# Performance work log

Measured on AMD Instinct MI355X. Metric: run time of the kernel, lower is better.

Reference implementation:

```python
import jax, jax.numpy as jnp
import numpy as np

NUM_CLASSES = 80
NUM_ANCHORS = 3
CONF_TH = 0.5
IOU_TH = 0.4
INPUT_H = 416
INPUT_W = 416
# anchors[i] used for scale i (scale1=stride8, scale2=stride16, scale3=stride32)
ANCHORS = np.array([[[10, 13], [16, 30], [33, 23]],
                    [[30, 61], [62, 45], [59, 119]],
                    [[116, 90], [156, 198], [373, 326]]], dtype=np.float32)


def setup_inputs() -> dict:
    key = jax.random.key(0)
    k1, k2, k3 = jax.random.split(key, 3)
    B = 4
    C = NUM_ANCHORS * (5 + NUM_CLASSES)  # 255
    return {
        'scale1': jax.random.normal(k1, (B, C, 52, 52), dtype=jnp.float32),
        'scale2': jax.random.normal(k2, (B, C, 26, 26), dtype=jnp.float32),
        'scale3': jax.random.normal(k3, (B, C, 13, 13), dtype=jnp.float32),
    }


def _decode(feat, anchors_s):
    # feat: [B, 3*(5+nc), H, W]; matches torch transpose(1,3)+reshape ordering
    B, C, H, W = feat.shape
    bbox_size = C // NUM_ANCHORS
    p = jnp.transpose(feat, (0, 3, 2, 1)).reshape(B, W * H * NUM_ANCHORS, bbox_size)
    xy = jax.nn.sigmoid(p[..., :2])
    conf_cls = jax.nn.sigmoid(p[..., 4:])
    # grid offsets: flat index = w*(H*3) + h*3 + a, offset = (w, h)
    ww, hh = jnp.meshgrid(jnp.arange(W), jnp.arange(H), indexing='ij')  # [W,H]
    cxy = jnp.stack([ww, hh], axis=-1).astype(p.dtype)                  # [W,H,2]
    cxy = jnp.broadcast_to(cxy[:, :, None, :], (W, H, NUM_ANCHORS, 2)).reshape(-1, 2)
    xy = xy + cxy                                                        # [B,N,2]
    anch = jnp.tile(anchors_s.astype(p.dtype), (H * W, 1))               # [N,2], anchor fastest
    wh = jnp.exp(p[..., 2:4]) * anch
    sx = float(INPUT_W // W)
    sy = float(INPUT_H // H)
    scale = jnp.array([sx, sy], dtype=p.dtype)
    xy = xy * scale
    wh = wh * scale
    return jnp.concatenate([xy, wh, conf_cls], axis=-1)  # [B,N,5+nc]


def _nms_image(d):
    # d: [N, 5+nc] decoded predictions for one image
    conf = d[:, 4]
    # bbox columns as in the original: [x-w/2, x+w/2, y-h/2, y+h/2]
    b0 = d[:, 0] - d[:, 2] * 0.5
    b1 = d[:, 0] + d[:, 2] * 0.5
    b2 = d[:, 1] - d[:, 3] * 0.5
    b3 = d[:, 1] + d[:, 3] * 0.5
    cls = jnp.argmax(d[:, 5:], axis=1)
    # bbox_iou reads columns as (xmin, ymin, xmax, ymax) = (b0, b1, b2, b3)
    area = jnp.clip(b2 - b0 + 1.0, 0.0) * jnp.clip(b3 - b1 + 1.0, 0.0)  # [N]
    ixmin = jnp.maximum(b0[:, None], b0[None, :])
    iymin = jnp.maximum(b1[:, None], b1[None, :])
    ixmax = jnp.minimum(b2[:, None], b2[None, :])
    iymax = jnp.minimum(b3[:, None], b3[None, :])
    inter = jnp.clip(ixmax - ixmin + 1.0, 0.0) * jnp.clip(iymax - iymin + 1.0, 0.0)
    iou = inter / (area[:, None] + area[None, :] - inter)  # [N,N]
    valid = conf > CONF_TH
    # faithful to the original masks (including comparing against only valid boxes)
    supp = (iou > IOU_TH) & (cls[:, None] == cls[None, :]) & (conf[:, None] < conf[None, :])
    supp = supp & valid[None, :]
    keep = valid & jnp.any(supp, axis=1)
    det = jnp.stack([b0, b1, b2, b3, conf, cls.astype(d.dtype)], axis=1)  # [N,6]
    return det, keep


def reference(scale1, scale2, scale3):
    d1 = _decode(scale1, jnp.asarray(ANCHORS[0]))
    d2 = _decode(scale2, jnp.asarray(ANCHORS[1]))
    d3 = _decode(scale3, jnp.asarray(ANCHORS[2]))
    decoded = jnp.concatenate([d1, d2, d3], axis=1)  # [B, N, 85]
    # sequential over batch to avoid materializing B NxN IoU matrices at once
    det, keep = jax.lax.map(_nms_image, decoded)     # [B,N,6], [B,N] bool
    return det, keep
```

## Files before the change

### kernel.cpp

```cpp
#include <hip/hip_runtime.h>
#include <math.h>

#define NDET 10647
#define NB 4
#define NCLS 80
#define CAP 160

__device__ __forceinline__ float sigmoidf_ref(float x) {
    if (x >= 0.f) {
        return 1.f / (1.f + expf(-x));
    } else {
        float e = expf(x);
        return e / (1.f + e);
    }
}

template <int S>
__device__ __forceinline__ void decode_cell(
    const float* __restrict__ feat, int b, int a, int cell, int off, float sx,
    float anchw, float anchh, float* __restrict__ det, float* __restrict__ keep,
    int* __restrict__ counts, float4* __restrict__ bbox,
    float* __restrict__ bconf, int* __restrict__ bidx)
{
    const int SS = S * S;
    const int h = cell / S;
    const int w = cell - h * S;
    const float* p = feat + ((size_t)(b * 255 + a * 85)) * SS + cell;

    float t0 = p[0 * SS];
    float t1 = p[1 * SS];
    float t2 = p[2 * SS];
    float t3 = p[3 * SS];
    float t4 = p[4 * SS];

#define CHAIN20(MV, IV, BASE)                                          \
    {                                                                  \
        float vv[20];                                                  \
        _Pragma("unroll")                                              \
        for (int j = 0; j < 20; ++j)                                   \
            vv[j] = p[(size_t)(5 + (BASE) + j) * SS];                  \
        MV = vv[0]; IV = (BASE);                                       \
        _Pragma("unroll")                                              \
        for (int j = 1; j < 20; ++j)                                   \
            if (vv[j] > MV) { MV = vv[j]; IV = (BASE) + j; }           \
    }

    float m0, m1, m2, m3;
    int i0, i1, i2, i3;
    CHAIN20(m0, i0, 0)
    CHAIN20(m1, i1, 20)
    CHAIN20(m2, i2, 40)
    CHAIN20(m3, i3, 60)
#undef CHAIN20

    float best = m0; int cls = i0;
    if (m1 > best) { best = m1; cls = i1; }
    if (m2 > best) { best = m2; cls = i2; }
    if (m3 > best) { best = m3; cls = i3; }

    float x  = (sigmoidf_ref(t0) + (float)w) * sx;
    float y  = (sigmoidf_ref(t1) + (float)h) * sx;
    float bw = expf(t2) * anchw * sx;
    float bh = expf(t3) * anchh * sx;
    float conf = sigmoidf_ref(t4);

    float b0 = x - bw * 0.5f;
    float b1 = x + bw * 0.5f;
    float b2 = y - bh * 0.5f;
    float b3 = y + bh * 0.5f;

    const int n = off + (w * S + h) * 3 + a;
    float2* o = reinterpret_cast<float2*>(det + ((size_t)b * NDET + n) * 6);
    o[0] = make_float2(b0, b1);
    o[1] = make_float2(b2, b3);
    o[2] = make_float2(conf, (float)cls);

    if (conf > 0.5f) {
        int bk = b * NCLS + cls;
        int pos = atomicAdd(&counts[bk], 1);
        if (pos < CAP) {
            int slot = bk * CAP + pos;
            bbox[slot]  = make_float4(b0, b1, b2, b3);
            bconf[slot] = conf;
            bidx[slot]  = n;
        }
    } else {
        keep[(size_t)b * NDET + n] = 0.f;
    }
}

__global__ __launch_bounds__(256, 1) void decode_kernel(
    const float* __restrict__ f0, const float* __restrict__ f1,
    const float* __restrict__ f2, float* __restrict__ det,
    float* __restrict__ keep, int* __restrict__ counts,
    float4* __restrict__ bbox, float* __restrict__ bconf, int* __restrict__ bidx)
{
    const int b = blockIdx.z;
    const int a = blockIdx.y;
    const int cx = blockIdx.x;
    const int tid = threadIdx.x;

    if (cx < 11) {
        int cell = cx * 256 + tid;
        if (cell < 52 * 52) {
            const float aw[3] = {10.f, 16.f, 33.f}, ah[3] = {13.f, 30.f, 23.f};
            decode_cell<52>(f0, b, a, cell, 0, 8.f, aw[a], ah[a],
                            det, keep, counts, bbox, bconf, bidx);
        }
    } else if (cx < 14) {
        int cell = (cx - 11) * 256 + tid;
        if (cell < 26 * 26) {
            const float aw[3] = {30.f, 62.f, 59.f}, ah[3] = {61.f, 45.f, 119.f};
            decode_cell<26>(f1, b, a, cell, 8112, 16.f, aw[a], ah[a],
                            det, keep, counts, bbox, bconf, bidx);
        }
    } else {
        int cell = tid;
        if (cell < 13 * 13) {
            const float aw[3] = {116.f, 156.f, 373.f}, ah[3] = {90.f, 198.f, 326.f};
            decode_cell<13>(f2, b, a, cell, 10140, 32.f, aw[a], ah[a],
                            det, keep, counts, bbox, bconf, bidx);
        }
    }
}

__global__ __launch_bounds__(192) void nms_kernel(
    const int* __restrict__ counts, const float4* __restrict__ bbox,
    const float* __restrict__ bconf, const int* __restrict__ bidx,
    float* __restrict__ keep)
{
    const int bk = blockIdx.x;
    const int b = bk / NCLS;
    int cnt = counts[bk];
    if (cnt > CAP) cnt = CAP;

    __shared__ float4 sb[CAP];
    __shared__ float  sc[CAP];
    __shared__ int    si[CAP];
    const int t = threadIdx.x;
    if (t < cnt) {
        sb[t] = bbox[bk * CAP + t];
        sc[t] = bconf[bk * CAP + t];
        si[t] = bidx[bk * CAP + t];
    }
    __syncthreads();
    if (t >= cnt) return;

    float4 me = sb[t];
    float ci = sc[t];
    float ai = fmaxf(me.z - me.x + 1.f, 0.f) * fmaxf(me.w - me.y + 1.f, 0.f);
    float kv = 0.f;
    for (int j = 0; j < cnt; ++j) {
        float cj = sc[j];
        float4 c = sb[j];
        float xmin = fmaxf(me.x, c.x);
        float ymin = fmaxf(me.y, c.y);
        float xmax = fminf(me.z, c.z);
        float ymax = fminf(me.w, c.w);
        float inter = fmaxf(xmax - xmin + 1.f, 0.f) * fmaxf(ymax - ymin + 1.f, 0.f);
        float aj = fmaxf(c.z - c.x + 1.f, 0.f) * fmaxf(c.w - c.y + 1.f, 0.f);
        float iou = inter / (ai + aj - inter);
        if (cj > ci && iou > 0.4f) kv = 1.f;
    }
    keep[(size_t)b * NDET + si[t]] = kv;
}

extern "C" void kernel_launch(void* const* d_in, const int* in_sizes, int n_in,
                              void* d_out, int out_size, void* d_ws, size_t ws_size,
                              hipStream_t stream) {
    const float* f0 = (const float*)d_in[0];
    const float* f1 = (const float*)d_in[1];
    const float* f2 = (const float*)d_in[2];
    float* det  = (float*)d_out;
    float* keep = det + (size_t)NB * NDET * 6;

    char* ws = (char*)d_ws;
    int* counts = (int*)ws;                             ws += NB * NCLS * sizeof(int);
    ws = (char*)(((uintptr_t)ws + 15) & ~(uintptr_t)15);
    float4* bbox = (float4*)ws;                         ws += (size_t)NB * NCLS * CAP * sizeof(float4);
    float* bconf = (float*)ws;                          ws += (size_t)NB * NCLS * CAP * sizeof(float);
    int*   bidx  = (int*)ws;

    hipMemsetAsync(counts, 0, NB * NCLS * sizeof(int), stream);

    dim3 gdec(15, 3, NB);
    hipLaunchKernelGGL(decode_kernel, gdec, dim3(256), 0, stream,
                       f0, f1, f2, det, keep, counts, bbox, bconf, bidx);

    hipLaunchKernelGGL(nms_kernel, dim3(NB * NCLS), dim3(192), 0, stream,
                       counts, bbox, bconf, bidx, keep);
}
```

Measured before the change: 33.79 us.

## Fuse decode and per-class NMS into one cooperative kernel with grid sync

Merges the decode and NMS kernels into a single cooperative launch separated by a grid-wide sync, removing the memset and a second launch. Decode now writes a compact conf/class array instead of appending to per-class buckets with global atomics. Each NMS block then rescans its whole image's conf/class array to gather its class's candidates in shared memory and rereads boxes from the det output. This trades launch and atomic overhead for redundant global/L2 scanning and grid-sync cost.

```diff
diff --git a/kernel.cpp b/kernel.cpp
--- a/kernel.cpp
+++ b/kernel.cpp
@@ -1,10 +1,15 @@
 #include <hip/hip_runtime.h>
+#include <hip/hip_cooperative_groups.h>
 #include <math.h>
+
+namespace cg = cooperative_groups;
 
 #define NDET 10647
 #define NB 4
 #define NCLS 80
 #define CAP 160
+#define NBLK 320
+#define NTHR 256
 
 __device__ __forceinline__ float sigmoidf_ref(float x) {
     if (x >= 0.f) {
@@ -19,8 +24,7 @@
 __device__ __forceinline__ void decode_cell(
     const float* __restrict__ feat, int b, int a, int cell, int off, float sx,
     float anchw, float anchh, float* __restrict__ det, float* __restrict__ keep,
-    int* __restrict__ counts, float4* __restrict__ bbox,
-    float* __restrict__ bconf, int* __restrict__ bidx)
+    float2* __restrict__ cc)
 {
     const int SS = S * S;
     const int h = cell / S;
@@ -75,84 +79,77 @@
     o[1] = make_float2(b2, b3);
     o[2] = make_float2(conf, (float)cls);
 
-    if (conf > 0.5f) {
-        int bk = b * NCLS + cls;
-        int pos = atomicAdd(&counts[bk], 1);
-        if (pos < CAP) {
-            int slot = bk * CAP + pos;
-            bbox[slot]  = make_float4(b0, b1, b2, b3);
-            bconf[slot] = conf;
-            bidx[slot]  = n;
-        }
-    } else {
-        keep[(size_t)b * NDET + n] = 0.f;
-    }
+    cc[(size_t)b * NDET + n] = make_float2(conf, (float)cls);
+    if (!(conf > 0.5f)) keep[(size_t)b * NDET + n] = 0.f;
 }
 
-__global__ __launch_bounds__(256, 1) void decode_kernel(
+__global__ __launch_bounds__(256, 2) void fused_kernel(
     const float* __restrict__ f0, const float* __restrict__ f1,
     const float* __restrict__ f2, float* __restrict__ det,
-    float* __restrict__ keep, int* __restrict__ counts,
-    float4* __restrict__ bbox, float* __restrict__ bconf, int* __restrict__ bidx)
+    float* __restrict__ keep, float2* __restrict__ cc)
 {
-    const int b = blockIdx.z;
-    const int a = blockIdx.y;
-    const int cx = blockIdx.x;
+    const int bx = blockIdx.x;
     const int tid = threadIdx.x;
 
-    if (cx < 11) {
-        int cell = cx * 256 + tid;
-        if (cell < 52 * 52) {
+    const int t = bx * NTHR + tid;
+    if (t < NB * 3 * 3549) {
+        const int ba = t / 3549;
+        const int cf = t - ba * 3549;
+        const int b = ba / 3;
+        const int a = ba - b * 3;
+        if (cf < 2704) {
             const float aw[3] = {10.f, 16.f, 33.f}, ah[3] = {13.f, 30.f, 23.f};
-            decode_cell<52>(f0, b, a, cell, 0, 8.f, aw[a], ah[a],
-                            det, keep, counts, bbox, bconf, bidx);
-        }
-    } else if (cx < 14) {
-        int cell = (cx - 11) * 256 + tid;
-        if (cell < 26 * 26) {
+            decode_cell<52>(f0, b, a, cf, 0, 8.f, aw[a], ah[a], det, keep, cc);
+        } else if (cf < 3380) {
             const float aw[3] = {30.f, 62.f, 59.f}, ah[3] = {61.f, 45.f, 119.f};
-            decode_cell<26>(f1, b, a, cell, 8112, 16.f, aw[a], ah[a],
-                            det, keep, counts, bbox, bconf, bidx);
-        }
-    } else {
-        int cell = tid;
-        if (cell < 13 * 13) {
+            decode_cell<26>(f1, b, a, cf - 2704, 8112, 16.f, aw[a], ah[a], det, keep, cc);
+        } else {
             const float aw[3] = {116.f, 156.f, 373.f}, ah[3] = {90.f, 198.f, 326.f};
-            decode_cell<13>(f2, b, a, cell, 10140, 32.f, aw[a], ah[a],
-                            det, keep, counts, bbox, bconf, bidx);
+            decode_cell<13>(f2, b, a, cf - 3380, 10140, 32.f, aw[a], ah[a], det, keep, cc);
         }
     }
-}
 
-__global__ __launch_bounds__(192) void nms_kernel(
-    const int* __restrict__ counts, const float4* __restrict__ bbox,
-    const float* __restrict__ bconf, const int* __restrict__ bidx,
-    float* __restrict__ keep)
-{
-    const int bk = blockIdx.x;
-    const int b = bk / NCLS;
-    int cnt = counts[bk];
+    cg::this_grid().sync();
+
+    const int b = bx / NCLS;
+    const float clsf = (float)(bx - b * NCLS);
+
+    __shared__ int   lcnt;
+    __shared__ int   si[CAP];
+    __shared__ float sc[CAP];
+    __shared__ float4 sbox[CAP];
+    if (tid == 0) lcnt = 0;
+    __syncthreads();
+
+    const float2* ccb = cc + (size_t)b * NDET;
+    for (int i = tid; i < NDET; i += NTHR) {
+        float2 v = ccb[i];
+        if (v.x > 0.5f && v.y == clsf) {
+            int k = atomicAdd(&lcnt, 1);
+            if (k < CAP) { si[k] = i; sc[k] = v.x; }
+        }
+    }
+    __syncthreads();
+    int cnt = lcnt;
     if (cnt > CAP) cnt = CAP;
 
-    __shared__ float4 sb[CAP];
-    __shared__ float  sc[CAP];
-    __shared__ int    si[CAP];
-    const int t = threadIdx.x;
-    if (t < cnt) {
-        sb[t] = bbox[bk * CAP + t];
-        sc[t] = bconf[bk * CAP + t];
-        si[t] = bidx[bk * CAP + t];
+    if (tid < cnt) {
+        const float2* dr = reinterpret_cast<const float2*>(
+            det + ((size_t)b * NDET + si[tid]) * 6);
+        float2 d0 = dr[0];
+        float2 d1 = dr[1];
+        sbox[tid] = make_float4(d0.x, d0.y, d1.x, d1.y);
     }
     __syncthreads();
-    if (t >= cnt) return;
+    if (tid >= cnt) return;
 
-    float4 me = sb[t];
-    float ci = sc[t];
+    float4 me = sbox[tid];
+    float ci = sc[tid];
     float ai = fmaxf(me.z - me.x + 1.f, 0.f) * fmaxf(me.w - me.y + 1.f, 0.f);
     float kv = 0.f;
     for (int j = 0; j < cnt; ++j) {
         float cj = sc[j];
-        float4 c = sb[j];
+        float4 c = sbox[j];
         float xmin = fmaxf(me.x, c.x);
         float ymin = fmaxf(me.y, c.y);
         float xmax = fminf(me.z, c.z);
@@ -162,7 +159,7 @@
         float iou = inter / (ai + aj - inter);
         if (cj > ci && iou > 0.4f) kv = 1.f;
     }
-    keep[(size_t)b * NDET + si[t]] = kv;
+    keep[(size_t)b * NDET + si[tid]] = kv;
 }
 
 extern "C" void kernel_launch(void* const* d_in, const int* in_sizes, int n_in,
@@ -173,20 +170,10 @@
     const float* f2 = (const float*)d_in[2];
     float* det  = (float*)d_out;
     float* keep = det + (size_t)NB * NDET * 6;
+    float2* cc  = (float2*)d_ws;
 
-    char* ws = (char*)d_ws;
-    int* counts = (int*)ws;                             ws += NB * NCLS * sizeof(int);
-    ws = (char*)(((uintptr_t)ws + 15) & ~(uintptr_t)15);
-    float4* bbox = (float4*)ws;                         ws += (size_t)NB * NCLS * CAP * sizeof(float4);
-    float* bconf = (float*)ws;                          ws += (size_t)NB * NCLS * CAP * sizeof(float);
-    int*   bidx  = (int*)ws;
-
-    hipMemsetAsync(counts, 0, NB * NCLS * sizeof(int), stream);
-
-    dim3 gdec(15, 3, NB);
-    hipLaunchKernelGGL(decode_kernel, gdec, dim3(256), 0, stream,
-                       f0, f1, f2, det, keep, counts, bbox, bconf, bidx);
-
-    hipLaunchKernelGGL(nms_kernel, dim3(NB * NCLS), dim3(192), 0, stream,
-                       counts, bbox, bconf, bidx, keep);
+    void* args[] = { (void*)&f0, (void*)&f1, (void*)&f2,
+                     (void*)&det, (void*)&keep, (void*)&cc };
+    hipLaunchCooperativeKernel((const void*)fused_kernel, dim3(NBLK), dim3(NTHR),
+                               args, 0, stream);
 }
```

New measurement: 81.41 us. 141% more time.
